# Optimization experiments

Hardware: AMD Instinct MI355X
Metric: run time of the kernel (lower is better)

## Reference

```python
import jax, jax.numpy as jnp
import numpy as np

EPS = 1e-8


def setup_inputs() -> dict:
    key = jax.random.key(0)
    k1, k2, k3, k4, k5 = jax.random.split(key, 5)
    N, B, T, D = 8, 2, 2048, 2048
    F = 4 * D
    blocks = jax.random.normal(k1, (N, B, T, D), dtype=jnp.float32)
    partial_block = jax.random.normal(k2, (B, T, D), dtype=jnp.float32)
    proj_w = jax.random.normal(k3, (D,), dtype=jnp.float32) * 0.02
    norm_scale = jnp.ones((D,), dtype=jnp.float32)
    ffn_w1 = jax.random.normal(k4, (D, F), dtype=jnp.float32) * 0.02
    ffn_w2 = jax.random.normal(k5, (F, D), dtype=jnp.float32) * 0.02
    return {
        "blocks": blocks,
        "partial_block": partial_block,
        "proj_w": proj_w,
        "norm_scale": norm_scale,
        "ffn_w1": ffn_w1,
        "ffn_w2": ffn_w2,
    }


def reference(blocks, partial_block, proj_w, norm_scale, ffn_w1, ffn_w2):
    # Stack completed blocks with current partial sum: V [N1, B, T, D]
    V = jnp.concatenate([blocks, partial_block[None]], axis=0)
    # RMSNorm over D (keys)
    rms = jnp.sqrt(jnp.mean(V * V, axis=-1, keepdims=True) + EPS)
    K = norm_scale * V / rms
    # Pseudo-query dot-product logits [N1, B, T], softmax over blocks (axis 0)
    logits = jnp.einsum('nbtd,d->nbt', K, proj_w)
    alpha = jax.nn.softmax(logits, axis=0)
    # Weighted sum of raw values -> new hidden state h [B, T, D]
    h = jnp.einsum('nbt,nbtd->btd', alpha, V)
    # Sublayer: standard FFN (D -> 4D gelu -> D)
    f_out = jax.nn.gelu(h @ ffn_w1) @ ffn_w2
    # layer_number % block_size != 0 branch: accumulate partial sum
    new_partial = partial_block + f_out
    return h, new_partial
```

## Files before the change

kernel.cpp:

```cpp
#include <hip/hip_runtime.h>

typedef unsigned short ushort_t;
typedef __bf16 bf16x8 __attribute__((ext_vector_type(8)));
typedef float f32x4 __attribute__((ext_vector_type(4)));

#define NB 8
#define BB 2
#define TT 2048
#define DD 2048
#define FF 8192
#define MM (BB * TT)
#define BTD ((size_t)BB * TT * DD)

__device__ __forceinline__ unsigned short f2bf(float f) {
  unsigned int u = __float_as_uint(f);
  u += 0x7FFFu + ((u >> 16) & 1u);
  return (unsigned short)(u >> 16);
}

__device__ __forceinline__ float gelu_tanh(float x) {
  float u = 0.7978845608028654f * (x + 0.044715f * x * x * x);
  float e = __expf(2.0f * u);
  float th = 1.0f - 2.0f / (e + 1.0f);
  return 0.5f * x * (1.0f + th);
}

template <int N>
__device__ __forceinline__ void wait_vmcnt() {
  if constexpr (N == 0) asm volatile("s_waitcnt vmcnt(0)" ::: "memory");
  else if constexpr (N == 3) asm volatile("s_waitcnt vmcnt(3)" ::: "memory");
  else if constexpr (N == 4) asm volatile("s_waitcnt vmcnt(4)" ::: "memory");
  else if constexpr (N == 6) asm volatile("s_waitcnt vmcnt(6)" ::: "memory");
  else if constexpr (N == 8) asm volatile("s_waitcnt vmcnt(8)" ::: "memory");
}

#define ASYNC_COPY16(gp, lp)                                                   \
  __builtin_amdgcn_global_load_lds(                                            \
      (__attribute__((address_space(1))) void*)(gp),                           \
      (__attribute__((address_space(3))) void*)(lp), 16, 0, 0)

__global__ __launch_bounds__(256) void transpose_conv(
    const float* __restrict__ in, ushort_t* __restrict__ out, int R, int C) {
  __shared__ float tile[32][33];
  const int tx = threadIdx.x & 31, ty = threadIdx.x >> 5;
  const int r0 = blockIdx.y * 32, c0 = blockIdx.x * 32;
#pragma unroll
  for (int i = 0; i < 32; i += 8)
    tile[ty + i][tx] = in[(size_t)(r0 + ty + i) * C + (c0 + tx)];
  __syncthreads();
#pragma unroll
  for (int i = 0; i < 32; i += 8)
    out[(size_t)(c0 + ty + i) * R + (r0 + tx)] = f2bf(tile[tx][ty + i]);
}

__global__ __launch_bounds__(256) void attn_fuse(
    const float* __restrict__ blocks, const float* __restrict__ partial,
    const float* __restrict__ proj_w, const float* __restrict__ norm_scale,
    float* __restrict__ h_out, ushort_t* __restrict__ h_bf) {
  const int t = threadIdx.x;
  const int bt = blockIdx.x;
  const size_t rowoff = (size_t)bt * DD;
  const int d0 = t * 4;

  float w[8];
  {
    float4 ns = *(const float4*)(norm_scale + d0);
    float4 pw = *(const float4*)(proj_w + d0);
    w[0] = ns.x * pw.x; w[1] = ns.y * pw.y; w[2] = ns.z * pw.z; w[3] = ns.w * pw.w;
    ns = *(const float4*)(norm_scale + 1024 + d0);
    pw = *(const float4*)(proj_w + 1024 + d0);
    w[4] = ns.x * pw.x; w[5] = ns.y * pw.y; w[6] = ns.z * pw.z; w[7] = ns.w * pw.w;
  }

  float vv[9][8];
  float ss[9], dt[9];
#pragma unroll
  for (int n = 0; n < 9; ++n) {
    const float* rp = (n < 8) ? (blocks + (size_t)n * BTD + rowoff)
                              : (partial + rowoff);
    float4 v0 = *(const float4*)(rp + d0);
    float4 v1 = *(const float4*)(rp + 1024 + d0);
    vv[n][0] = v0.x; vv[n][1] = v0.y; vv[n][2] = v0.z; vv[n][3] = v0.w;
    vv[n][4] = v1.x; vv[n][5] = v1.y; vv[n][6] = v1.z; vv[n][7] = v1.w;
    float a = 0.f, c = 0.f;
#pragma unroll
    for (int j = 0; j < 8; ++j) {
      a += vv[n][j] * vv[n][j];
      c += vv[n][j] * w[j];
    }
    ss[n] = a; dt[n] = c;
  }

  __shared__ float red[2][9][4];
  const int lane = t & 63, wv = t >> 6;
#pragma unroll
  for (int n = 0; n < 9; ++n) {
    float a = ss[n], c = dt[n];
#pragma unroll
    for (int off = 32; off > 0; off >>= 1) {
      a += __shfl_down(a, off, 64);
      c += __shfl_down(c, off, 64);
    }
    if (lane == 0) { red[0][n][wv] = a; red[1][n][wv] = c; }
  }
  __syncthreads();
  __shared__ float logit_s[9];
  if (t < 9) {
    float a = red[0][t][0] + red[0][t][1] + red[0][t][2] + red[0][t][3];
    float c = red[1][t][0] + red[1][t][1] + red[1][t][2] + red[1][t][3];
    logit_s[t] = c * rsqrtf(a * (1.0f / (float)DD) + 1e-8f);
  }
  __syncthreads();

  float lg[9], mx = -1e30f;
#pragma unroll
  for (int n = 0; n < 9; ++n) { lg[n] = logit_s[n]; mx = fmaxf(mx, lg[n]); }
  float den = 0.0f;
#pragma unroll
  for (int n = 0; n < 9; ++n) { lg[n] = __expf(lg[n] - mx); den += lg[n]; }
  const float inv = 1.0f / den;

  float h[8] = {0, 0, 0, 0, 0, 0, 0, 0};
#pragma unroll
  for (int n = 0; n < 9; ++n) {
    const float a = lg[n] * inv;
#pragma unroll
    for (int j = 0; j < 8; ++j) h[j] += a * vv[n][j];
  }

  float4 o0 = {h[0], h[1], h[2], h[3]}, o1 = {h[4], h[5], h[6], h[7]};
  *(float4*)(h_out + rowoff + d0) = o0;
  *(float4*)(h_out + rowoff + 1024 + d0) = o1;
  uint2 p0, p1;
  p0.x = (unsigned)f2bf(h[0]) | ((unsigned)f2bf(h[1]) << 16);
  p0.y = (unsigned)f2bf(h[2]) | ((unsigned)f2bf(h[3]) << 16);
  p1.x = (unsigned)f2bf(h[4]) | ((unsigned)f2bf(h[5]) << 16);
  p1.y = (unsigned)f2bf(h[6]) | ((unsigned)f2bf(h[7]) << 16);
  *(uint2*)(h_bf + rowoff + d0) = p0;
  *(uint2*)(h_bf + rowoff + 1024 + d0) = p1;
}

template <int BN, int WM, int WN, int SBY, int SBX, int MCX, int EPI>
__global__ __launch_bounds__(512, 2) void gemmQ(
    const ushort_t* __restrict__ A, const ushort_t* __restrict__ BT,
    const int K, const int N, ushort_t* __restrict__ Cb,
    const float* __restrict__ addend, float* __restrict__ Cf) {
  constexpr int MFR = 256 / WM / 16;
  constexpr int NFR = BN / WN / 16;
  constexpr int AS = 16384;
  constexpr int BS = BN * 64;
  constexpr int RS = AS + BS;
  constexpr int LB = BS / 8192;
  constexpr int LT = 2 + LB;

  __shared__ __align__(16) char lds[4 * RS];

  const int t = threadIdx.x;
  const int lane = t & 63, wv = t >> 6;
  const int fr = lane & 15, kslot = lane >> 4;
  const int WRow = (wv / WN) * (256 / WM);
  const int WCol = (wv % WN) * (BN / WN);

  const int wg = blockIdx.x;
  const int xcd = wg & 7, local = wg >> 3;
  const int by = (xcd / MCX) * SBY + local / SBX;
  const int bx = (xcd % MCX) * SBX + local % SBX;
  const int row0 = by * 256, col0 = bx * BN;

  const ushort_t* ga[2];
  const ushort_t* gb[LB];
#pragma unroll
  for (int j = 0; j < 2; ++j) {
    const int o = j * 8192 + t * 16;
    const int rp = o >> 7;
    const int iX = (o & 127) ^ ((rp & 7) << 4);
    ga[j] = A + (size_t)(row0 + rp * 2 + (iX >> 6)) * K + ((iX & 63) >> 1);
  }
#pragma unroll
  for (int j = 0; j < LB; ++j) {
    const int o = j * 8192 + t * 16;
    const int rp = o >> 7;
    const int iX = (o & 127) ^ ((rp & 7) << 4);
    gb[j] = BT + (size_t)(col0 + rp * 2 + (iX >> 6)) * K + ((iX & 63) >> 1);
  }

#define STAGE(QQ, KT)                                                          \
  {                                                                            \
    ASYNC_COPY16(ga[0] + (size_t)(KT) * 32, lds + (QQ)*RS + t * 16);           \
    ASYNC_COPY16(ga[1] + (size_t)(KT) * 32, lds + (QQ)*RS + 8192 + t * 16);    \
    ASYNC_COPY16(gb[0] + (size_t)(KT) * 32, lds + (QQ)*RS + AS + t * 16);      \
    if constexpr (LB == 2)                                                     \
      ASYNC_COPY16(gb[1] + (size_t)(KT) * 32,                                  \
                   lds + (QQ)*RS + AS + 8192 + t * 16);                        \
  }

  const int arp0 = (WRow + fr) >> 1;
  const int aoff =
      arp0 * 128 + (((((fr & 1) << 6) | (kslot << 4))) ^ ((arp0 & 7) << 4));
  const int brp0 = (WCol + fr) >> 1;
  const int boff = AS + brp0 * 128 +
                   (((((fr & 1) << 6) | (kslot << 4))) ^ ((brp0 & 7) << 4));

  f32x4 acc[MFR][NFR];
#pragma unroll
  for (int m = 0; m < MFR; ++m)
#pragma unroll
    for (int n = 0; n < NFR; ++n) {
      f32x4 z = {0.f, 0.f, 0.f, 0.f};
      acc[m][n] = z;
    }

#define MFMA_(a, b, c) __builtin_amdgcn_mfma_f32_16x16x32_bf16(a, b, c, 0, 0, 0)

  const int NT = K >> 5;

  STAGE(0, 0);
  STAGE(1, 1);
  STAGE(2, 2);
  wait_vmcnt<LT>();
  __builtin_amdgcn_s_barrier();

  bf16x8 bs0[NFR], bs1[NFR];
#pragma unroll
  for (int n = 0; n < NFR; ++n)
    bs0[n] = *(const bf16x8*)(lds + boff + n * 1024);

#define INTERVAL(QQ, KT, BCUR, BNXT)                                           \
  {                                                                            \
    if ((KT) + 3 < NT) STAGE(((QQ) + 3) & 3, (KT) + 3);                        \
    const char* Lq = lds + (QQ)*RS;                                            \
    const char* Ln = lds + (((QQ) + 1) & 3) * RS;                              \
    bf16x8 af[MFR];                                                            \
    _Pragma("unroll") for (int m = 0; m < MFR; ++m)                            \
      af[m] = *(const bf16x8*)(Lq + aoff + m * 1024);                          \
    if ((KT) + 1 < NT) {                                                       \
      _Pragma("unroll") for (int n = 0; n < NFR; ++n)                          \
        BNXT[n] = *(const bf16x8*)(Ln + boff + n * 1024);                      \
    }                                                                          \
    __builtin_amdgcn_s_setprio(1);                                             \
    _Pragma("unroll") for (int m = 0; m < MFR; ++m)                            \
      _Pragma("unroll") for (int n = 0; n < NFR; ++n)                          \
        acc[m][n] = MFMA_(af[m], BCUR[n], acc[m][n]);                          \
    __builtin_amdgcn_s_setprio(0);                                             \
    if ((KT) + 3 < NT) wait_vmcnt<LT>(); else wait_vmcnt<0>();                 \
    __builtin_amdgcn_s_barrier();                                              \
  }

  for (int t0 = 0; t0 < NT; t0 += 4) {
    INTERVAL(0, t0 + 0, bs0, bs1);
    INTERVAL(1, t0 + 1, bs1, bs0);
    INTERVAL(2, t0 + 2, bs0, bs1);
    INTERVAL(3, t0 + 3, bs1, bs0);
  }

  const int r4 = kslot * 4;
#pragma unroll
  for (int m = 0; m < MFR; ++m) {
    const int grow = row0 + WRow + m * 16 + r4;
#pragma unroll
    for (int n = 0; n < NFR; ++n) {
      const int gcol = col0 + WCol + n * 16 + fr;
#pragma unroll
      for (int r = 0; r < 4; ++r) {
        const float v = acc[m][n][r];
        const size_t idx = (size_t)(grow + r) * N + gcol;
        if (EPI == 0) {
          Cb[idx] = f2bf(gelu_tanh(v));
        } else {
          Cf[idx] = v + addend[idx];
        }
      }
    }
  }
#undef INTERVAL
#undef MFMA_
#undef STAGE
}

extern "C" void kernel_launch(void* const* d_in, const int* in_sizes, int n_in,
                              void* d_out, int out_size, void* d_ws,
                              size_t ws_size, hipStream_t stream) {
  const float* blocks = (const float*)d_in[0];
  const float* partial = (const float*)d_in[1];
  const float* proj_w = (const float*)d_in[2];
  const float* norm_scale = (const float*)d_in[3];
  const float* w1 = (const float*)d_in[4];
  const float* w2 = (const float*)d_in[5];

  float* out = (float*)d_out;
  float* h_out = out;
  float* new_partial = out + BTD;

  char* ws = (char*)d_ws;
  ushort_t* h_bf = (ushort_t*)ws;
  ushort_t* w1T = (ushort_t*)(ws + (size_t)16777216);
  ushort_t* w2T = (ushort_t*)(ws + (size_t)16777216 + 33554432);
  ushort_t* act = (ushort_t*)(ws + (size_t)16777216 + 2 * 33554432ull);

  transpose_conv<<<dim3(FF / 32, DD / 32), 256, 0, stream>>>(w1, w1T, DD, FF);
  transpose_conv<<<dim3(DD / 32, FF / 32), 256, 0, stream>>>(w2, w2T, FF, DD);

  attn_fuse<<<MM, 256, 0, stream>>>(blocks, partial, proj_w, norm_scale, h_out,
                                    h_bf);

  gemmQ<256, 2, 4, 8, 8, 4, 0><<<512, 512, 0, stream>>>(
      h_bf, w1T, DD, FF, act, nullptr, nullptr);
  gemmQ<128, 4, 2, 4, 8, 2, 1><<<256, 512, 0, stream>>>(
      act, w2T, FF, DD, nullptr, partial, new_partial);
}
```

Baseline: 398.9 us.

## Use 4-wave 256-thread GEMM with larger per-wave tiles and full A/B double-buffering

Replaces the 8-wave 512-thread GEMM with a 4-wave 256-thread kernel where each wave computes a 128-row by BN/2 tile. Both A and B fragments for the next k-step are now prefetched from LDS into registers, not just B. The aim is more MFMA work per LDS read and better latency hiding. The cost is heavier register use, one workgroup per CU with fewer waves, and twice as many async copies per thread per stage.

```diff
diff --git a/kernel.cpp b/kernel.cpp
--- a/kernel.cpp
+++ b/kernel.cpp
@@ -28,8 +28,6 @@
 template <int N>
 __device__ __forceinline__ void wait_vmcnt() {
   if constexpr (N == 0) asm volatile("s_waitcnt vmcnt(0)" ::: "memory");
-  else if constexpr (N == 3) asm volatile("s_waitcnt vmcnt(3)" ::: "memory");
-  else if constexpr (N == 4) asm volatile("s_waitcnt vmcnt(4)" ::: "memory");
   else if constexpr (N == 6) asm volatile("s_waitcnt vmcnt(6)" ::: "memory");
   else if constexpr (N == 8) asm volatile("s_waitcnt vmcnt(8)" ::: "memory");
 }
@@ -140,26 +138,27 @@
   *(uint2*)(h_bf + rowoff + 1024 + d0) = p1;
 }
 
-template <int BN, int WM, int WN, int SBY, int SBX, int MCX, int EPI>
-__global__ __launch_bounds__(512, 2) void gemmQ(
+template <int BN, int SBY, int SBX, int MCX, int EPI>
+__global__ __launch_bounds__(256, 1) void gemmP(
     const ushort_t* __restrict__ A, const ushort_t* __restrict__ BT,
     const int K, const int N, ushort_t* __restrict__ Cb,
     const float* __restrict__ addend, float* __restrict__ Cf) {
-  constexpr int MFR = 256 / WM / 16;
-  constexpr int NFR = BN / WN / 16;
+  constexpr int MFR = 8;
+  constexpr int NFR = BN / 32;
   constexpr int AS = 16384;
   constexpr int BS = BN * 64;
   constexpr int RS = AS + BS;
-  constexpr int LB = BS / 8192;
-  constexpr int LT = 2 + LB;
+  constexpr int LA = 4;
+  constexpr int LBN = BS / 4096;
+  constexpr int LT = LA + LBN;
 
   __shared__ __align__(16) char lds[4 * RS];
 
   const int t = threadIdx.x;
   const int lane = t & 63, wv = t >> 6;
   const int fr = lane & 15, kslot = lane >> 4;
-  const int WRow = (wv / WN) * (256 / WM);
-  const int WCol = (wv % WN) * (BN / WN);
+  const int WRow = (wv >> 1) * 128;
+  const int WCol = (wv & 1) * (BN / 2);
 
   const int wg = blockIdx.x;
   const int xcd = wg & 7, local = wg >> 3;
@@ -167,18 +166,18 @@
   const int bx = (xcd % MCX) * SBX + local % SBX;
   const int row0 = by * 256, col0 = bx * BN;
 
-  const ushort_t* ga[2];
-  const ushort_t* gb[LB];
-#pragma unroll
-  for (int j = 0; j < 2; ++j) {
-    const int o = j * 8192 + t * 16;
+  const ushort_t* ga[LA];
+  const ushort_t* gb[LBN];
+#pragma unroll
+  for (int j = 0; j < LA; ++j) {
+    const int o = j * 4096 + t * 16;
     const int rp = o >> 7;
     const int iX = (o & 127) ^ ((rp & 7) << 4);
     ga[j] = A + (size_t)(row0 + rp * 2 + (iX >> 6)) * K + ((iX & 63) >> 1);
   }
 #pragma unroll
-  for (int j = 0; j < LB; ++j) {
-    const int o = j * 8192 + t * 16;
+  for (int j = 0; j < LBN; ++j) {
+    const int o = j * 4096 + t * 16;
     const int rp = o >> 7;
     const int iX = (o & 127) ^ ((rp & 7) << 4);
     gb[j] = BT + (size_t)(col0 + rp * 2 + (iX >> 6)) * K + ((iX & 63) >> 1);
@@ -186,12 +185,12 @@
 
 #define STAGE(QQ, KT)                                                          \
   {                                                                            \
-    ASYNC_COPY16(ga[0] + (size_t)(KT) * 32, lds + (QQ)*RS + t * 16);           \
-    ASYNC_COPY16(ga[1] + (size_t)(KT) * 32, lds + (QQ)*RS + 8192 + t * 16);    \
-    ASYNC_COPY16(gb[0] + (size_t)(KT) * 32, lds + (QQ)*RS + AS + t * 16);      \
-    if constexpr (LB == 2)                                                     \
-      ASYNC_COPY16(gb[1] + (size_t)(KT) * 32,                                  \
-                   lds + (QQ)*RS + AS + 8192 + t * 16);                        \
+    _Pragma("unroll") for (int j = 0; j < LA; ++j)                             \
+      ASYNC_COPY16(ga[j] + (size_t)(KT) * 32,                                  \
+                   lds + (QQ)*RS + j * 4096 + t * 16);                         \
+    _Pragma("unroll") for (int j = 0; j < LBN; ++j)                            \
+      ASYNC_COPY16(gb[j] + (size_t)(KT) * 32,                                  \
+                   lds + (QQ)*RS + AS + j * 4096 + t * 16);                    \
   }
 
   const int arp0 = (WRow + fr) >> 1;
@@ -201,6 +200,16 @@
   const int boff = AS + brp0 * 128 +
                    (((((fr & 1) << 6) | (kslot << 4))) ^ ((brp0 & 7) << 4));
 
+  bf16x8 a0[MFR], b0[NFR], a1[MFR], b1[NFR];
+
+#define READF(AX, BX, Lb)                                                      \
+  {                                                                            \
+    _Pragma("unroll") for (int m = 0; m < MFR; ++m)                            \
+      AX[m] = *(const bf16x8*)((Lb) + aoff + m * 1024);                        \
+    _Pragma("unroll") for (int n = 0; n < NFR; ++n)                            \
+      BX[n] = *(const bf16x8*)((Lb) + boff + n * 1024);                        \
+  }
+
   f32x4 acc[MFR][NFR];
 #pragma unroll
   for (int m = 0; m < MFR; ++m)
@@ -211,6 +220,22 @@
     }
 
 #define MFMA_(a, b, c) __builtin_amdgcn_mfma_f32_16x16x32_bf16(a, b, c, 0, 0, 0)
+
+#define INTERVAL(QQ, KT, AC, BC, AN, BNX)                                      \
+  {                                                                            \
+    if ((KT) + 3 < NT) STAGE(((QQ) + 3) & 3, (KT) + 3);                        \
+    if ((KT) + 1 < NT) {                                                       \
+      const char* Ln = lds + (((QQ) + 1) & 3) * RS;                            \
+      READF(AN, BNX, Ln);                                                      \
+    }                                                                          \
+    __builtin_amdgcn_s_setprio(1);                                             \
+    _Pragma("unroll") for (int m = 0; m < MFR; ++m)                            \
+      _Pragma("unroll") for (int n = 0; n < NFR; ++n)                          \
+        acc[m][n] = MFMA_(AC[m], BC[n], acc[m][n]);                            \
+    __builtin_amdgcn_s_setprio(0);                                             \
+    if ((KT) + 3 < NT) wait_vmcnt<LT>(); else wait_vmcnt<0>();                 \
+    __builtin_amdgcn_s_barrier();                                              \
+  }
 
   const int NT = K >> 5;
 
@@ -219,38 +244,13 @@
   STAGE(2, 2);
   wait_vmcnt<LT>();
   __builtin_amdgcn_s_barrier();
-
-  bf16x8 bs0[NFR], bs1[NFR];
-#pragma unroll
-  for (int n = 0; n < NFR; ++n)
-    bs0[n] = *(const bf16x8*)(lds + boff + n * 1024);
-
-#define INTERVAL(QQ, KT, BCUR, BNXT)                                           \
-  {                                                                            \
-    if ((KT) + 3 < NT) STAGE(((QQ) + 3) & 3, (KT) + 3);                        \
-    const char* Lq = lds + (QQ)*RS;                                            \
-    const char* Ln = lds + (((QQ) + 1) & 3) * RS;                              \
-    bf16x8 af[MFR];                                                            \
-    _Pragma("unroll") for (int m = 0; m < MFR; ++m)                            \
-      af[m] = *(const bf16x8*)(Lq + aoff + m * 1024);                          \
-    if ((KT) + 1 < NT) {                                                       \
-      _Pragma("unroll") for (int n = 0; n < NFR; ++n)                          \
-        BNXT[n] = *(const bf16x8*)(Ln + boff + n * 1024);                      \
-    }                                                                          \
-    __builtin_amdgcn_s_setprio(1);                                             \
-    _Pragma("unroll") for (int m = 0; m < MFR; ++m)                            \
-      _Pragma("unroll") for (int n = 0; n < NFR; ++n)                          \
-        acc[m][n] = MFMA_(af[m], BCUR[n], acc[m][n]);                          \
-    __builtin_amdgcn_s_setprio(0);                                             \
-    if ((KT) + 3 < NT) wait_vmcnt<LT>(); else wait_vmcnt<0>();                 \
-    __builtin_amdgcn_s_barrier();                                              \
-  }
+  READF(a0, b0, (const char*)lds);
 
   for (int t0 = 0; t0 < NT; t0 += 4) {
-    INTERVAL(0, t0 + 0, bs0, bs1);
-    INTERVAL(1, t0 + 1, bs1, bs0);
-    INTERVAL(2, t0 + 2, bs0, bs1);
-    INTERVAL(3, t0 + 3, bs1, bs0);
+    INTERVAL(0, t0 + 0, a0, b0, a1, b1);
+    INTERVAL(1, t0 + 1, a1, b1, a0, b0);
+    INTERVAL(2, t0 + 2, a0, b0, a1, b1);
+    INTERVAL(3, t0 + 3, a1, b1, a0, b0);
   }
 
   const int r4 = kslot * 4;
@@ -274,6 +274,7 @@
   }
 #undef INTERVAL
 #undef MFMA_
+#undef READF
 #undef STAGE
 }
 
@@ -303,8 +304,8 @@
   attn_fuse<<<MM, 256, 0, stream>>>(blocks, partial, proj_w, norm_scale, h_out,
                                     h_bf);
 
-  gemmQ<256, 2, 4, 8, 8, 4, 0><<<512, 512, 0, stream>>>(
+  gemmP<256, 8, 8, 4, 0><<<512, 256, 0, stream>>>(
       h_bf, w1T, DD, FF, act, nullptr, nullptr);
-  gemmQ<128, 4, 2, 4, 8, 2, 1><<<256, 512, 0, stream>>>(
+  gemmP<128, 4, 8, 2, 1><<<256, 256, 0, stream>>>(
       act, w2T, FF, DD, nullptr, partial, new_partial);
 }
```

New measurement: 437.9 us. 9.8% more time.
